# Kernel tuning notes

Hardware: AMD Instinct MI355X
Metric: run time of the kernel (lower is better)

Reference implementation:

```python
import jax, jax.numpy as jnp
import numpy as np

DIM = 1024
NQ = 16
NKV = 4
HD = DIM // NQ  # 64
HID = 2048
E = 8
B, S = 1, 1024
EPS = 1e-6


def rmsnorm(x, w):
    ms = jnp.mean(x * x, axis=-1, keepdims=True)
    return w * (x * jax.lax.rsqrt(ms + EPS))


def rope_tables(seq_len, head_dim):
    inv_freq = 1.0 / (10000.0 ** (jnp.arange(0, head_dim, 2, dtype=jnp.float32) / head_dim))
    t = jnp.arange(seq_len, dtype=jnp.float32)
    freqs = jnp.einsum('i,j->ij', t, inv_freq)  # [S, HD/2]
    return jnp.cos(freqs), jnp.sin(freqs)


def apply_rope(x, cos, sin):
    # x: [B, S, H, HD]; cos/sin: [S, HD/2]
    c = cos[None, :, None, :]
    s = sin[None, :, None, :]
    half = x.shape[-1] // 2
    x1, x2 = x[..., :half], x[..., half:]
    return jnp.concatenate([x1 * c - x2 * s, x1 * s + x2 * c], axis=-1)


def setup_inputs() -> dict:
    key = jax.random.key(0)
    ks = jax.random.split(key, 20)
    sc = lambda fan_in: 1.0 / np.sqrt(fan_in)
    d = {}
    d['x'] = jax.random.normal(ks[0], (B, S, DIM), dtype=jnp.float32)
    d['ln1_w'] = jnp.ones((DIM,), jnp.float32)
    d['ln2_w'] = jnp.ones((DIM,), jnp.float32)
    d['Wq'] = jax.random.normal(ks[1], (DIM, DIM), jnp.float32) * sc(DIM)
    d['bq'] = jnp.zeros((DIM,), jnp.float32)
    d['Wk'] = jax.random.normal(ks[2], (DIM, HD * NKV), jnp.float32) * sc(DIM)
    d['bk'] = jnp.zeros((HD * NKV,), jnp.float32)
    d['Wv'] = jax.random.normal(ks[3], (DIM, HD * NKV), jnp.float32) * sc(DIM)
    d['bv'] = jnp.zeros((HD * NKV,), jnp.float32)
    d['qn_w'] = jnp.ones((HD,), jnp.float32)
    d['kn_w'] = jnp.ones((HD,), jnp.float32)
    d['Wg'] = jax.random.normal(ks[4], (HD, HD), jnp.float32) * sc(HD)
    d['bg'] = jnp.zeros((HD,), jnp.float32)
    d['Wo'] = jax.random.normal(ks[5], (DIM, DIM), jnp.float32) * sc(DIM)
    d['bo'] = jnp.zeros((DIM,), jnp.float32)
    d['Wr'] = jax.random.normal(ks[6], (DIM, E), jnp.float32) * sc(DIM)
    d['br'] = jnp.zeros((E,), jnp.float32)
    d['W1'] = jax.random.normal(ks[7], (E, DIM, 2 * HID), jnp.float32) * sc(DIM)
    d['b1'] = jnp.zeros((E, 2 * HID), jnp.float32)
    d['W2'] = jax.random.normal(ks[8], (E, HID, DIM), jnp.float32) * sc(HID)
    d['b2'] = jnp.zeros((E, DIM), jnp.float32)
    return d


def _forward(x, ln1_w, ln2_w, Wq, bq, Wk, bk, Wv, bv, qn_w, kn_w, Wg, bg, Wo, bo,
             Wr, br, W1, b1, W2, b2):
    batch, seq, _ = x.shape
    cos, sin = rope_tables(seq, HD)

    # --- attention ---
    h = rmsnorm(x, ln1_w)
    q = (h @ Wq + bq).reshape(batch, seq, NQ, HD)
    k = (h @ Wk + bk).reshape(batch, seq, NKV, HD)
    v = (h @ Wv + bv).reshape(batch, seq, NKV, HD)
    q = rmsnorm(apply_rope(q, cos, sin), qn_w)
    k = rmsnorm(apply_rope(k, cos, sin), kn_w)
    rep = NQ // NKV
    k = jnp.repeat(k, rep, axis=2)  # [B,S,NQ,HD]
    v = jnp.repeat(v, rep, axis=2)
    scores = jnp.einsum('bthd,bshd->bhts', q, k) / np.sqrt(HD)
    causal = jnp.tril(jnp.ones((seq, seq), dtype=bool))
    scores = jnp.where(causal[None, None], scores, -jnp.inf)
    attn = jax.nn.softmax(scores, axis=-1)
    out = jnp.einsum('bhts,bshd->bthd', attn, v)
    gate = jax.nn.sigmoid(out @ Wg + bg)
    out = (out * gate).reshape(batch, seq, DIM)
    x = x + out @ Wo + bo

    # --- top-1 MoE (note: output is NOT scaled by router probs) ---
    h2 = rmsnorm(x, ln2_w)
    logits = h2 @ Wr + br  # [B,S,E]
    top1 = jnp.argmax(logits, axis=-1).reshape(-1)  # [T]
    xt = h2.reshape(-1, DIM)  # [T,DIM]
    # dense dispatch: run all experts, gather the chosen one
    u = jnp.einsum('td,edf->tef', xt, W1) + b1  # [T,E,2H]
    u1, u2 = u[..., :HID], u[..., HID:]
    act = u1 * jax.nn.sigmoid(u2)  # SwiGLU
    y_all = jnp.einsum('teh,ehd->ted', act, W2) + b2  # [T,E,DIM]
    y = jnp.take_along_axis(y_all, top1[:, None, None], axis=1)[:, 0, :]
    return x + y.reshape(batch, seq, DIM)


def reference(x, ln1_w, ln2_w, Wq, bq, Wk, bk, Wv, bv, qn_w, kn_w, Wg, bg, Wo, bo,
              Wr, br, W1, b1, W2, b2):
    return _forward(x, ln1_w, ln2_w, Wq, bq, Wk, bk, Wv, bv, qn_w, kn_w,
                    Wg, bg, Wo, bo, Wr, br, W1, b1, W2, b2)
```

## Files before the change

kernel.cpp:

```cpp
#include <hip/hip_runtime.h>
#include <hip/hip_bf16.h>
#include <cstddef>

#define DIM 1024
#define NQ 16
#define NKV 4
#define HD 64
#define HID 2048
#define NE 8
#define SEQ 1024
#define EPSF 1e-6f
#define MAX_TILES 24
#define GST 72

typedef __hip_bfloat16 bf16;
typedef __attribute__((ext_vector_type(8))) short short8;
typedef __attribute__((ext_vector_type(4))) float floatx4;

typedef union { short8 s; unsigned int u[4]; } s8u;

__device__ __forceinline__ unsigned int f2b(float f) {
    union { bf16 b; unsigned short s; } u;
    u.b = __float2bfloat16(f);
    return (unsigned int)u.s;
}
__device__ __forceinline__ unsigned int pk2(float a, float b) {
    return f2b(a) | (f2b(b) << 16);
}

__global__ __launch_bounds__(256) void rmsnorm_kernel(const float* __restrict__ src,
                                                      const float* __restrict__ w,
                                                      float* __restrict__ dst)
{
    int row = blockIdx.x, tid = threadIdx.x;
    __shared__ float red[256];
    float vals[4];
    float sq = 0.f;
    size_t base = (size_t)row * DIM;
    #pragma unroll
    for (int i = 0; i < 4; i++) {
        int idx = tid + i * 256;
        float v = src[base + idx];
        vals[i] = v; sq += v * v;
    }
    red[tid] = sq; __syncthreads();
    for (int s = 128; s > 0; s >>= 1) {
        if (tid < s) red[tid] += red[tid + s];
        __syncthreads();
    }
    float rs = 1.0f / sqrtf(red[0] * (1.0f / DIM) + EPSF);
    #pragma unroll
    for (int i = 0; i < 4; i++) {
        int idx = tid + i * 256;
        dst[base + idx] = w[idx] * vals[i] * rs;
    }
}

__global__ __launch_bounds__(256) void gemm_kernel(
    const float* __restrict__ A, const float* __restrict__ B, const float* __restrict__ bias,
    float* __restrict__ C, const float* __restrict__ resf,
    const int* __restrict__ perm, const int* __restrict__ tile_expert,
    int N, int K, int mode)
{
    __shared__ short As[64 * GST];
    __shared__ short Bs[64 * GST];
    int tid = threadIdx.x;
    int mbase = blockIdx.y * 64, nbase = blockIdx.x * 64;

    size_t Beoff = 0, biasoff = 0;
    if (tile_expert) {
        int e = tile_expert[blockIdx.y];
        if (e < 0) return;
        Beoff = (size_t)e * K * N;
        biasoff = (size_t)e * N;
    }

    int ar = tid >> 4, ak = (tid & 15) << 2;
    int bn = tid & 63, bkk = (tid >> 6) << 4;
    const float* BpBase = B + Beoff + (size_t)bkk * N + nbase + bn;

    int wv = tid >> 6, ln = tid & 63;
    int fm = (wv << 4) + (ln & 15);
    int fn = ln & 15;
    int fk = (ln >> 4) << 3;

    floatx4 acc[4];
    #pragma unroll
    for (int nt = 0; nt < 4; nt++)
        #pragma unroll
        for (int r = 0; r < 4; r++) acc[nt][r] = 0.f;

    float4 apre[4];
    float bpre[16];
    #pragma unroll
    for (int p = 0; p < 4; p++)
        apre[p] = *(const float4*)(A + (size_t)(mbase + (p << 4) + ar) * K + ak);
    #pragma unroll
    for (int i = 0; i < 16; i++)
        bpre[i] = BpBase[(size_t)i * N];

    for (int kt = 0; kt < K; kt += 64) {
        #pragma unroll
        for (int p = 0; p < 4; p++) {
            int m = (p << 4) + ar;
            uint2 wpk; wpk.x = pk2(apre[p].x, apre[p].y); wpk.y = pk2(apre[p].z, apre[p].w);
            *(uint2*)&As[m * GST + ak] = wpk;
        }
        {
            unsigned int u[8];
            #pragma unroll
            for (int i = 0; i < 8; i++) u[i] = pk2(bpre[2 * i], bpre[2 * i + 1]);
            *(uint4*)&Bs[bn * GST + bkk]     = make_uint4(u[0], u[1], u[2], u[3]);
            *(uint4*)&Bs[bn * GST + bkk + 8] = make_uint4(u[4], u[5], u[6], u[7]);
        }
        __syncthreads();

        int kn = kt + 64;
        if (kn < K) {
            #pragma unroll
            for (int p = 0; p < 4; p++)
                apre[p] = *(const float4*)(A + (size_t)(mbase + (p << 4) + ar) * K + kn + ak);
            const float* bp = BpBase + (size_t)kn * N;
            #pragma unroll
            for (int i = 0; i < 16; i++) bpre[i] = bp[(size_t)i * N];
        }

        #pragma unroll
        for (int ks = 0; ks < 2; ks++) {
            short8 af = *(const short8*)&As[fm * GST + (ks << 5) + fk];
            #pragma unroll
            for (int nt = 0; nt < 4; nt++) {
                short8 bf = *(const short8*)&Bs[((nt << 4) + fn) * GST + (ks << 5) + fk];
                acc[nt] = __builtin_amdgcn_mfma_f32_16x16x32_bf16(af, bf, acc[nt], 0, 0, 0);
            }
        }
        __syncthreads();
    }

    int rowb = mbase + (wv << 4) + ((ln >> 4) << 2);
    if (mode == 2) {
        int tk[4];
        #pragma unroll
        for (int r = 0; r < 4; r++) tk[r] = perm[rowb + r];
        #pragma unroll
        for (int nt = 0; nt < 4; nt++) {
            int col = nbase + (nt << 4) + fn;
            float bsv = bias[biasoff + col];
            #pragma unroll
            for (int r = 0; r < 4; r++)
                if (tk[r] >= 0)
                    C[(size_t)tk[r] * N + col] = resf[(size_t)tk[r] * N + col] + acc[nt][r] + bsv;
        }
    } else {
        #pragma unroll
        for (int nt = 0; nt < 4; nt++) {
            int col = nbase + (nt << 4) + fn;
            float bsv = bias[col];
            #pragma unroll
            for (int r = 0; r < 4; r++) {
                float vv = acc[nt][r] + bsv;
                if (mode == 1) vv += resf[(size_t)(rowb + r) * N + col];
                C[(size_t)(rowb + r) * N + col] = vv;
            }
        }
    }
}

__global__ __launch_bounds__(256) void qkv_kernel(
    const float* __restrict__ A,
    const float* __restrict__ Wq, const float* __restrict__ bq,
    const float* __restrict__ Wk, const float* __restrict__ bk,
    const float* __restrict__ Wv, const float* __restrict__ bv,
    float* __restrict__ qo, float* __restrict__ ko, float* __restrict__ vo)
{
    __shared__ short As[64 * GST];
    __shared__ short Bs[64 * GST];
    int tid = threadIdx.x;
    int bx = blockIdx.x;
    int mbase = blockIdx.y * 64;

    const float* B; const float* bias; float* C; int N, nbase;
    if (bx < 16)      { B = Wq; bias = bq; C = qo; N = DIM;      nbase = bx * 64; }
    else if (bx < 20) { B = Wk; bias = bk; C = ko; N = NKV * HD; nbase = (bx - 16) * 64; }
    else              { B = Wv; bias = bv; C = vo; N = NKV * HD; nbase = (bx - 20) * 64; }

    int ar = tid >> 4, ak = (tid & 15) << 2;
    int bn = tid & 63, bkk = (tid >> 6) << 4;
    const float* BpBase = B + (size_t)bkk * N + nbase + bn;

    int wv = tid >> 6, ln = tid & 63;
    int fm = (wv << 4) + (ln & 15);
    int fn = ln & 15;
    int fk = (ln >> 4) << 3;

    floatx4 acc[4];
    #pragma unroll
    for (int nt = 0; nt < 4; nt++)
        #pragma unroll
        for (int r = 0; r < 4; r++) acc[nt][r] = 0.f;

    float4 apre[4];
    float bpre[16];
    #pragma unroll
    for (int p = 0; p < 4; p++)
        apre[p] = *(const float4*)(A + (size_t)(mbase + (p << 4) + ar) * DIM + ak);
    #pragma unroll
    for (int i = 0; i < 16; i++)
        bpre[i] = BpBase[(size_t)i * N];

    for (int kt = 0; kt < DIM; kt += 64) {
        #pragma unroll
        for (int p = 0; p < 4; p++) {
            int m = (p << 4) + ar;
            uint2 wpk; wpk.x = pk2(apre[p].x, apre[p].y); wpk.y = pk2(apre[p].z, apre[p].w);
            *(uint2*)&As[m * GST + ak] = wpk;
        }
        {
            unsigned int u[8];
            #pragma unroll
            for (int i = 0; i < 8; i++) u[i] = pk2(bpre[2 * i], bpre[2 * i + 1]);
            *(uint4*)&Bs[bn * GST + bkk]     = make_uint4(u[0], u[1], u[2], u[3]);
            *(uint4*)&Bs[bn * GST + bkk + 8] = make_uint4(u[4], u[5], u[6], u[7]);
        }
        __syncthreads();

        int kn = kt + 64;
        if (kn < DIM) {
            #pragma unroll
            for (int p = 0; p < 4; p++)
                apre[p] = *(const float4*)(A + (size_t)(mbase + (p << 4) + ar) * DIM + kn + ak);
            const float* bp = BpBase + (size_t)kn * N;
            #pragma unroll
            for (int i = 0; i < 16; i++) bpre[i] = bp[(size_t)i * N];
        }

        #pragma unroll
        for (int ks = 0; ks < 2; ks++) {
            short8 af = *(const short8*)&As[fm * GST + (ks << 5) + fk];
            #pragma unroll
            for (int nt = 0; nt < 4; nt++) {
                short8 bf = *(const short8*)&Bs[((nt << 4) + fn) * GST + (ks << 5) + fk];
                acc[nt] = __builtin_amdgcn_mfma_f32_16x16x32_bf16(af, bf, acc[nt], 0, 0, 0);
            }
        }
        __syncthreads();
    }

    int rowb = mbase + (wv << 4) + ((ln >> 4) << 2);
    #pragma unroll
    for (int nt = 0; nt < 4; nt++) {
        int col = nbase + (nt << 4) + fn;
        float bsv = bias[col];
        #pragma unroll
        for (int r = 0; r < 4; r++)
            C[(size_t)(rowb + r) * N + col] = acc[nt][r] + bsv;
    }
}

__global__ __launch_bounds__(256) void moe1_kernel(
    const float* __restrict__ A,
    const float* __restrict__ W1,
    const float* __restrict__ b1,
    float* __restrict__ act,
    const int* __restrict__ perm,
    const int* __restrict__ tile_expert)
{
    __shared__ short As[64 * GST];
    __shared__ short B1s[64 * GST];
    __shared__ short B2s[64 * GST];
    int tid = threadIdx.x;
    int mbase = blockIdx.y * 64, nbase = blockIdx.x * 64;
    int e = tile_expert[blockIdx.y];
    if (e < 0) return;
    const float* Wp = W1 + (size_t)e * DIM * (2 * HID);
    const float* bp1 = b1 + (size_t)e * (2 * HID);

    int ar = tid >> 4, ak = (tid & 15) << 2;
    int tok[4];
    #pragma unroll
    for (int p = 0; p < 4; p++) tok[p] = perm[mbase + (p << 4) + ar];

    int bn = tid & 63, bkk = (tid >> 6) << 4;
    const float* BpBase = Wp + (size_t)bkk * (2 * HID) + nbase + bn;

    int wv = tid >> 6, ln = tid & 63;
    int fm = (wv << 4) + (ln & 15);
    int fn = ln & 15;
    int fk = (ln >> 4) << 3;

    floatx4 acc1[4], acc2[4];
    #pragma unroll
    for (int nt = 0; nt < 4; nt++)
        #pragma unroll
        for (int r = 0; r < 4; r++) { acc1[nt][r] = 0.f; acc2[nt][r] = 0.f; }

    float4 apre[4];
    float b1pre[16], b2pre[16];
    #pragma unroll
    for (int p = 0; p < 4; p++)
        apre[p] = (tok[p] >= 0)
            ? *(const float4*)(A + (size_t)tok[p] * DIM + ak)
            : make_float4(0.f, 0.f, 0.f, 0.f);
    #pragma unroll
    for (int i = 0; i < 16; i++) {
        b1pre[i] = BpBase[(size_t)i * (2 * HID)];
        b2pre[i] = BpBase[(size_t)i * (2 * HID) + HID];
    }

    for (int kt = 0; kt < DIM; kt += 64) {
        #pragma unroll
        for (int p = 0; p < 4; p++) {
            int m = (p << 4) + ar;
            uint2 wpk; wpk.x = pk2(apre[p].x, apre[p].y); wpk.y = pk2(apre[p].z, apre[p].w);
            *(uint2*)&As[m * GST + ak] = wpk;
        }
        {
            unsigned int u1[8], u2[8];
            #pragma unroll
            for (int i = 0; i < 8; i++) {
                u1[i] = pk2(b1pre[2 * i], b1pre[2 * i + 1]);
                u2[i] = pk2(b2pre[2 * i], b2pre[2 * i + 1]);
            }
            *(uint4*)&B1s[bn * GST + bkk]     = make_uint4(u1[0], u1[1], u1[2], u1[3]);
            *(uint4*)&B1s[bn * GST + bkk + 8] = make_uint4(u1[4], u1[5], u1[6], u1[7]);
            *(uint4*)&B2s[bn * GST + bkk]     = make_uint4(u2[0], u2[1], u2[2], u2[3]);
            *(uint4*)&B2s[bn * GST + bkk + 8] = make_uint4(u2[4], u2[5], u2[6], u2[7]);
        }
        __syncthreads();

        int kn = kt + 64;
        if (kn < DIM) {
            #pragma unroll
            for (int p = 0; p < 4; p++)
                apre[p] = (tok[p] >= 0)
                    ? *(const float4*)(A + (size_t)tok[p] * DIM + kn + ak)
                    : make_float4(0.f, 0.f, 0.f, 0.f);
            const float* bp = BpBase + (size_t)kn * (2 * HID);
            #pragma unroll
            for (int i = 0; i < 16; i++) {
                b1pre[i] = bp[(size_t)i * (2 * HID)];
                b2pre[i] = bp[(size_t)i * (2 * HID) + HID];
            }
        }

        #pragma unroll
        for (int ks = 0; ks < 2; ks++) {
            short8 af = *(const short8*)&As[fm * GST + (ks << 5) + fk];
            #pragma unroll
            for (int nt = 0; nt < 4; nt++) {
                int bo = ((nt << 4) + fn) * GST + (ks << 5) + fk;
                short8 bf1 = *(const short8*)&B1s[bo];
                short8 bf2 = *(const short8*)&B2s[bo];
                acc1[nt] = __builtin_amdgcn_mfma_f32_16x16x32_bf16(af, bf1, acc1[nt], 0, 0, 0);
                acc2[nt] = __builtin_amdgcn_mfma_f32_16x16x32_bf16(af, bf2, acc2[nt], 0, 0, 0);
            }
        }
        __syncthreads();
    }

    int rowb = mbase + (wv << 4) + ((ln >> 4) << 2);
    #pragma unroll
    for (int nt = 0; nt < 4; nt++) {
        int col = nbase + (nt << 4) + fn;
        float bs1 = bp1[col];
        float bs2 = bp1[HID + col];
        #pragma unroll
        for (int r = 0; r < 4; r++) {
            float u1 = acc1[nt][r] + bs1;
            float u2 = acc2[nt][r] + bs2;
            act[(size_t)(rowb + r) * HID + col] = u1 * (1.0f / (1.0f + expf(-u2)));
        }
    }
}

__global__ __launch_bounds__(64) void rope_rms_kernel(float* __restrict__ x,
                                                      const float* __restrict__ w, int nh)
{
    int t = blockIdx.x, h = blockIdx.y, d = threadIdx.x;
    int base = (t * nh + h) * HD;
    int i = d & 31;
    float x1 = x[base + i];
    float x2 = x[base + 32 + i];
    float inv = 1.0f / powf(10000.0f, (float)(2 * i) * (1.0f / HD));
    float fr = (float)t * inv;
    float c = cosf(fr), s = sinf(fr);
    float r = (d < 32) ? (x1 * c - x2 * s) : (x1 * s + x2 * c);
    float sq = r * r;
    #pragma unroll
    for (int m = 32; m >= 1; m >>= 1) sq += __shfl_xor(sq, m);
    float rs = 1.0f / sqrtf(sq * (1.0f / HD) + EPSF);
    __syncthreads();
    x[base + d] = r * rs * w[d];
}

__global__ __launch_bounds__(256) void fattn_kernel(const float* __restrict__ q,
                                                    const float* __restrict__ k,
                                                    const float* __restrict__ v,
                                                    float* __restrict__ o)
{
    __shared__ short lds[2][2][64 * GST];

    int h = blockIdx.x, qt = blockIdx.y;
    int kvh = h >> 2;
    int tid = threadIdx.x;
    int w = tid >> 6, ln = tid & 63;
    int c = ln & 15, g = ln >> 4;
    int qbase = qt * 64;
    const size_t krow = (size_t)NKV * HD;

    short8 qf[2];
    {
        const float* qp = q + ((size_t)(qbase + 16 * w + c) * NQ + h) * HD + 8 * g;
        #pragma unroll
        for (int ks = 0; ks < 2; ks++) {
            float4 a = *(const float4*)(qp + 32 * ks);
            float4 b = *(const float4*)(qp + 32 * ks + 4);
            s8u t;
            t.u[0] = pk2(a.x * 0.125f, a.y * 0.125f);
            t.u[1] = pk2(a.z * 0.125f, a.w * 0.125f);
            t.u[2] = pk2(b.x * 0.125f, b.y * 0.125f);
            t.u[3] = pk2(b.z * 0.125f, b.w * 0.125f);
            qf[ks] = t.s;
        }
    }

    int kr[4], kd4[4];
    #pragma unroll
    for (int i = 0; i < 4; i++) { int f4 = tid + 256 * i; kr[i] = f4 >> 4; kd4[i] = f4 & 15; }
    int vd = tid & 63, vrb = (tid >> 6) << 4;

    float4 kreg[4];
    float vreg[16];
    {
        const float* kb = k + (size_t)kvh * HD;
        #pragma unroll
        for (int i = 0; i < 4; i++)
            kreg[i] = *(const float4*)(kb + (size_t)kr[i] * krow + kd4[i] * 4);
        const float* vb = v + (size_t)kvh * HD + vd;
        #pragma unroll
        for (int i = 0; i < 16; i++)
            vreg[i] = vb[(size_t)(vrb + i) * krow];
    }

    float m_i = -INFINITY, l_i = 0.f;
    floatx4 ot[4];
    #pragma unroll
    for (int mt = 0; mt < 4; mt++)
        #pragma unroll
        for (int r = 0; r < 4; r++) ot[mt][r] = 0.f;

    for (int kt = 0; kt <= qt; kt++) {
        short* KB = lds[kt & 1][0];
        short* VT = lds[kt & 1][1];

        #pragma unroll
        for (int i = 0; i < 4; i++) {
            uint2 wp; wp.x = pk2(kreg[i].x, kreg[i].y); wp.y = pk2(kreg[i].z, kreg[i].w);
            *(uint2*)&KB[kr[i] * GST + kd4[i] * 4] = wp;
        }
        {
            unsigned int u[8];
            #pragma unroll
            for (int i = 0; i < 8; i++) u[i] = pk2(vreg[2 * i], vreg[2 * i + 1]);
            *(uint4*)&VT[vd * GST + vrb]     = make_uint4(u[0], u[1], u[2], u[3]);
            *(uint4*)&VT[vd * GST + vrb + 8] = make_uint4(u[4], u[5], u[6], u[7]);
        }
        __syncthreads();

        if (kt < qt) {
            int kb2 = (kt + 1) * 64;
            const float* kb = k + ((size_t)kb2 * NKV + kvh) * HD;
            #pragma unroll
            for (int i = 0; i < 4; i++)
                kreg[i] = *(const float4*)(kb + (size_t)kr[i] * krow + kd4[i] * 4);
            const float* vp = v + ((size_t)kb2 * NKV + kvh) * HD + vd;
            #pragma unroll
            for (int i = 0; i < 16; i++)
                vreg[i] = vp[(size_t)(vrb + i) * krow];
        }

        float p[4][4];
        #pragma unroll
        for (int mt = 0; mt < 4; mt++) {
            floatx4 s = {0.f, 0.f, 0.f, 0.f};
            #pragma unroll
            for (int ks = 0; ks < 2; ks++) {
                short8 kf = *(const short8*)&KB[(16 * mt + c) * GST + 32 * ks + 8 * g];
                s = __builtin_amdgcn_mfma_f32_16x16x32_bf16(kf, qf[ks], s, 0, 0, 0);
            }
            #pragma unroll
            for (int r = 0; r < 4; r++) p[mt][r] = s[r];
        }

        if (kt == qt) {
            #pragma unroll
            for (int mt = 0; mt < 4; mt++)
                #pragma unroll
                for (int r = 0; r < 4; r++)
                    if (16 * mt + 4 * g + r > 16 * w + c) p[mt][r] = -1e30f;
        }

        float tm = p[0][0];
        #pragma unroll
        for (int mt = 0; mt < 4; mt++)
            #pragma unroll
            for (int r = 0; r < 4; r++) tm = fmaxf(tm, p[mt][r]);
        tm = fmaxf(tm, __shfl_xor(tm, 16));
        tm = fmaxf(tm, __shfl_xor(tm, 32));
        float mn = fmaxf(m_i, tm);
        float alpha = __expf(m_i - mn);
        float ts = 0.f;
        #pragma unroll
        for (int mt = 0; mt < 4; mt++)
            #pragma unroll
            for (int r = 0; r < 4; r++) {
                float e = __expf(p[mt][r] - mn);
                p[mt][r] = e; ts += e;
            }
        ts += __shfl_xor(ts, 16);
        ts += __shfl_xor(ts, 32);
        l_i = alpha * l_i + ts;
        m_i = mn;
        #pragma unroll
        for (int mt = 0; mt < 4; mt++)
            #pragma unroll
            for (int r = 0; r < 4; r++) ot[mt][r] *= alpha;

        unsigned int pd[4][2];
        #pragma unroll
        for (int mt = 0; mt < 4; mt++) {
            pd[mt][0] = pk2(p[mt][0], p[mt][1]);
            pd[mt][1] = pk2(p[mt][2], p[mt][3]);
        }

        int srcA = c + ((ln & 16) << 1);
        int srcB = srcA + 16;
        int gh = g >> 1;
        short8 pf[2];
        #pragma unroll
        for (int ks = 0; ks < 2; ks++) {
            s8u t;
            unsigned int a0 = (unsigned)__shfl((int)pd[2 * ks][0],     srcA);
            unsigned int a1 = (unsigned)__shfl((int)pd[2 * ks + 1][0], srcA);
            t.u[0] = gh ? a1 : a0;
            unsigned int b0 = (unsigned)__shfl((int)pd[2 * ks][1],     srcA);
            unsigned int b1 = (unsigned)__shfl((int)pd[2 * ks + 1][1], srcA);
            t.u[1] = gh ? b1 : b0;
            unsigned int c0 = (unsigned)__shfl((int)pd[2 * ks][0],     srcB);
            unsigned int c1 = (unsigned)__shfl((int)pd[2 * ks + 1][0], srcB);
            t.u[2] = gh ? c1 : c0;
            unsigned int d0 = (unsigned)__shfl((int)pd[2 * ks][1],     srcB);
            unsigned int d1 = (unsigned)__shfl((int)pd[2 * ks + 1][1], srcB);
            t.u[3] = gh ? d1 : d0;
            pf[ks] = t.s;
        }

        #pragma unroll
        for (int mt = 0; mt < 4; mt++) {
            #pragma unroll
            for (int ks = 0; ks < 2; ks++) {
                short8 vf = *(const short8*)&VT[(16 * mt + c) * GST + 32 * ks + 8 * g];
                ot[mt] = __builtin_amdgcn_mfma_f32_16x16x32_bf16(vf, pf[ks], ot[mt], 0, 0, 0);
            }
        }
    }

    __syncthreads();
    float* OT = (float*)lds;
    float rl = 1.0f / l_i;
    #pragma unroll
    for (int mt = 0; mt < 4; mt++)
        #pragma unroll
        for (int r = 0; r < 4; r++)
            OT[(16 * w + c) * 68 + 16 * mt + 4 * g + r] = ot[mt][r] * rl;
    __syncthreads();
    #pragma unroll
    for (int i = 0; i < 4; i++) {
        int idx = tid + 256 * i;
        int rq = idx >> 4, d4 = idx & 15;
        float4 val = *(const float4*)&OT[rq * 68 + d4 * 4];
        *(float4*)(o + ((size_t)(qbase + rq) * NQ + h) * HD + d4 * 4) = val;
    }
}

__global__ __launch_bounds__(64) void gate_kernel(float* __restrict__ o,
                                                  const float* __restrict__ Wg,
                                                  const float* __restrict__ bg)
{
    int t = blockIdx.x, h = blockIdx.y, d = threadIdx.x;
    __shared__ float ao[HD];
    int base = (t * NQ + h) * HD;
    ao[d] = o[base + d];
    __syncthreads();
    float acc = bg[d];
    #pragma unroll 8
    for (int e = 0; e < HD; e++) acc += ao[e] * Wg[e * HD + d];
    float g = 1.0f / (1.0f + expf(-acc));
    o[base + d] = ao[d] * g;
}

__global__ __launch_bounds__(64) void router_kernel(const float* __restrict__ h2,
                                                    const float* __restrict__ Wr,
                                                    const float* __restrict__ br,
                                                    int* __restrict__ top1)
{
    int t = blockIdx.x, lane = threadIdx.x;
    float acc[NE] = {0.f, 0.f, 0.f, 0.f, 0.f, 0.f, 0.f, 0.f};
    for (int d = lane; d < DIM; d += 64) {
        float hv = h2[(size_t)t * DIM + d];
        float4 w0 = *(const float4*)(Wr + (size_t)d * NE);
        float4 w1 = *(const float4*)(Wr + (size_t)d * NE + 4);
        acc[0] += hv * w0.x; acc[1] += hv * w0.y;
        acc[2] += hv * w0.z; acc[3] += hv * w0.w;
        acc[4] += hv * w1.x; acc[5] += hv * w1.y;
        acc[6] += hv * w1.z; acc[7] += hv * w1.w;
    }
    #pragma unroll
    for (int e = 0; e < NE; e++)
        for (int off = 32; off >= 1; off >>= 1) acc[e] += __shfl_down(acc[e], off);
    if (lane == 0) {
        float best = acc[0] + br[0]; int be = 0;
        #pragma unroll
        for (int e = 1; e < NE; e++) {
            float l = acc[e] + br[e];
            if (l > best) { best = l; be = e; }
        }
        top1[t] = be;
    }
}

__global__ __launch_bounds__(64) void bucket_kernel(const int* __restrict__ top1,
                                                    int* __restrict__ perm,
                                                    int* __restrict__ tile_expert)
{
    int lane = threadIdx.x;

    int e_of[16];
    {
        const int4* tp = (const int4*)(top1 + lane * 16);
        #pragma unroll
        for (int c = 0; c < 4; c++) {
            int4 v = tp[c];
            e_of[c * 4 + 0] = v.x & 7;
            e_of[c * 4 + 1] = v.y & 7;
            e_of[c * 4 + 2] = v.z & 7;
            e_of[c * 4 + 3] = v.w & 7;
        }
    }

    int cnt[NE];
    #pragma unroll
    for (int e = 0; e < NE; e++) {
        int c = 0;
        #pragma unroll
        for (int i = 0; i < 16; i++) c += (e_of[i] == e) ? 1 : 0;
        cnt[e] = c;
    }

    int pre[NE];
    #pragma unroll
    for (int e = 0; e < NE; e++) pre[e] = cnt[e];
    #pragma unroll
    for (int off = 1; off < 64; off <<= 1) {
        #pragma unroll
        for (int e = 0; e < NE; e++) {
            int t = __shfl_up(pre[e], off);
            if (lane >= off) pre[e] += t;
        }
    }
    int tot[NE];
    #pragma unroll
    for (int e = 0; e < NE; e++) {
        tot[e] = __shfl(pre[e], 63);
        pre[e] -= cnt[e];
    }

    int off_e[NE + 1];
    off_e[0] = 0;
    #pragma unroll
    for (int e = 0; e < NE; e++)
        off_e[e + 1] = off_e[e] + (((tot[e] + 63) >> 6) << 6);

    if (lane < MAX_TILES) {
        int tb = lane << 6;
        int te = -1;
        #pragma unroll
        for (int e = 0; e < NE; e++)
            if (tb >= off_e[e] && tb < off_e[e + 1]) te = e;
        tile_expert[lane] = te;
    }

    #pragma unroll
    for (int e = 0; e < NE; e++)
        for (int i = off_e[e] + tot[e] + lane; i < off_e[e + 1]; i += 64)
            perm[i] = -1;

    #pragma unroll
    for (int e = 0; e < NE; e++) {
        int pos = off_e[e] + pre[e];
        #pragma unroll
        for (int i = 0; i < 16; i++) {
            if (e_of[i] == e) { perm[pos] = lane * 16 + i; pos++; }
        }
    }
}

extern "C" void kernel_launch(void* const* d_in, const int* in_sizes, int n_in,
                              void* d_out, int out_size, void* d_ws, size_t ws_size,
                              hipStream_t stream)
{
    const float* x    = (const float*)d_in[0];
    const float* ln1w = (const float*)d_in[1];
    const float* ln2w = (const float*)d_in[2];
    const float* Wq   = (const float*)d_in[3];
    const float* bq   = (const float*)d_in[4];
    const float* Wk   = (const float*)d_in[5];
    const float* bk   = (const float*)d_in[6];
    const float* Wv   = (const float*)d_in[7];
    const float* bv   = (const float*)d_in[8];
    const float* qnw  = (const float*)d_in[9];
    const float* knw  = (const float*)d_in[10];
    const float* Wg   = (const float*)d_in[11];
    const float* bg   = (const float*)d_in[12];
    const float* Wo   = (const float*)d_in[13];
    const float* bo   = (const float*)d_in[14];
    const float* Wr   = (const float*)d_in[15];
    const float* br   = (const float*)d_in[16];
    const float* W1   = (const float*)d_in[17];
    const float* b1   = (const float*)d_in[18];
    const float* W2   = (const float*)d_in[19];
    const float* b2   = (const float*)d_in[20];
    float* out = (float*)d_out;
    (void)in_sizes; (void)n_in; (void)out_size; (void)ws_size;

    char* ws = (char*)d_ws;
    float* h    = (float*)(ws);
    float* q    = (float*)(ws + ((size_t)4  << 20));
    float* kbuf = (float*)(ws + ((size_t)8  << 20));
    float* vbuf = (float*)(ws + ((size_t)9  << 20));
    float* ao   = (float*)(ws + ((size_t)10 << 20));
    float* x2   = (float*)(ws);
    float* h2   = (float*)(ws + ((size_t)4  << 20));
    float* act  = (float*)(ws + ((size_t)8  << 20));
    int* top1   = (int*)  (ws + ((size_t)20 << 20));
    int* perm   = top1 + 2048;
    int* texp   = perm + MAX_TILES * 64;

    rmsnorm_kernel<<<SEQ, 256, 0, stream>>>(x, ln1w, h);
    qkv_kernel<<<dim3(24, SEQ / 64), 256, 0, stream>>>(
        h, Wq, bq, Wk, bk, Wv, bv, q, kbuf, vbuf);
    rope_rms_kernel<<<dim3(SEQ, NQ),  64, 0, stream>>>(q,    qnw, NQ);
    rope_rms_kernel<<<dim3(SEQ, NKV), 64, 0, stream>>>(kbuf, knw, NKV);
    fattn_kernel<<<dim3(NQ, SEQ / 64), 256, 0, stream>>>(q, kbuf, vbuf, ao);
    gate_kernel<<<dim3(SEQ, NQ), 64, 0, stream>>>(ao, Wg, bg);
    gemm_kernel<<<dim3(DIM / 64, SEQ / 64), 256, 0, stream>>>(
        ao, Wo, bo, x2, x, nullptr, nullptr, DIM, DIM, 1);
    rmsnorm_kernel<<<SEQ, 256, 0, stream>>>(x2, ln2w, h2);
    router_kernel<<<SEQ, 64, 0, stream>>>(h2, Wr, br, top1);
    bucket_kernel<<<1, 64, 0, stream>>>(top1, perm, texp);
    moe1_kernel<<<dim3(HID / 64, MAX_TILES), 256, 0, stream>>>(
        h2, W1, b1, act, perm, texp);
    gemm_kernel<<<dim3(DIM / 64, MAX_TILES), 256, 0, stream>>>(
        act, W2, b2, out, x2, perm, texp, DIM, HID, 2);
}
```

Baseline: 436.9 us.

## Enlarge MoE tiles to 128 rows, fuse gate into attention, merge rope launches

Grows the MoE expert tiles from 64 to 128 token rows, so each W1/W2 weight tile loaded from memory feeds twice as many MFMAs. MoE2 gets its own gemm2 kernel and the bucket padding moves to 128 with 16 tiles. The sigmoid gate projection moves into the flash-attention epilogue, removing the separate gate kernel and its extra read and write of the attention output. The Q and K rope/rmsnorm launches become one. Risks: more padding waste per expert, higher register pressure from doubled accumulators, and extra serial work in the attention epilogue.

```diff
diff --git a/kernel.cpp b/kernel.cpp
--- a/kernel.cpp
+++ b/kernel.cpp
@@ -10,7 +10,7 @@
 #define NE 8
 #define SEQ 1024
 #define EPSF 1e-6f
-#define MAX_TILES 24
+#define MAX_TILES 16
 #define GST 72
 
 typedef __hip_bfloat16 bf16;
@@ -59,7 +59,6 @@
 __global__ __launch_bounds__(256) void gemm_kernel(
     const float* __restrict__ A, const float* __restrict__ B, const float* __restrict__ bias,
     float* __restrict__ C, const float* __restrict__ resf,
-    const int* __restrict__ perm, const int* __restrict__ tile_expert,
     int N, int K, int mode)
 {
     __shared__ short As[64 * GST];
@@ -67,17 +66,9 @@
     int tid = threadIdx.x;
     int mbase = blockIdx.y * 64, nbase = blockIdx.x * 64;
 
-    size_t Beoff = 0, biasoff = 0;
-    if (tile_expert) {
-        int e = tile_expert[blockIdx.y];
-        if (e < 0) return;
-        Beoff = (size_t)e * K * N;
-        biasoff = (size_t)e * N;
-    }
-
     int ar = tid >> 4, ak = (tid & 15) << 2;
     int bn = tid & 63, bkk = (tid >> 6) << 4;
-    const float* BpBase = B + Beoff + (size_t)bkk * N + nbase + bn;
+    const float* BpBase = B + (size_t)bkk * N + nbase + bn;
 
     int wv = tid >> 6, ln = tid & 63;
     int fm = (wv << 4) + (ln & 15);
@@ -138,30 +129,118 @@
     }
 
     int rowb = mbase + (wv << 4) + ((ln >> 4) << 2);
-    if (mode == 2) {
+    #pragma unroll
+    for (int nt = 0; nt < 4; nt++) {
+        int col = nbase + (nt << 4) + fn;
+        float bsv = bias[col];
+        #pragma unroll
+        for (int r = 0; r < 4; r++) {
+            float vv = acc[nt][r] + bsv;
+            if (mode == 1) vv += resf[(size_t)(rowb + r) * N + col];
+            C[(size_t)(rowb + r) * N + col] = vv;
+        }
+    }
+}
+
+__global__ __launch_bounds__(256) void gemm2_kernel(
+    const float* __restrict__ A,
+    const float* __restrict__ W2,
+    const float* __restrict__ b2,
+    float* __restrict__ C,
+    const float* __restrict__ resf,
+    const int* __restrict__ perm,
+    const int* __restrict__ tile_expert)
+{
+    __shared__ short As[128 * GST];
+    __shared__ short Bs[64 * GST];
+    int tid = threadIdx.x;
+    int mbase = blockIdx.y * 128, nbase = blockIdx.x * 64;
+    int e = tile_expert[blockIdx.y];
+    if (e < 0) return;
+    const int N = DIM, K = HID;
+    const float* Bp = W2 + (size_t)e * K * N;
+    const float* bias = b2 + (size_t)e * N;
+
+    int ar = tid >> 4, ak = (tid & 15) << 2;
+    int bn = tid & 63, bkk = (tid >> 6) << 4;
+    const float* BpBase = Bp + (size_t)bkk * N + nbase + bn;
+
+    int wv = tid >> 6, ln = tid & 63;
+    int fm = (wv << 4) + (ln & 15);
+    int fn = ln & 15;
+    int fk = (ln >> 4) << 3;
+
+    floatx4 acc[2][4];
+    #pragma unroll
+    for (int ms = 0; ms < 2; ms++)
+        #pragma unroll
+        for (int nt = 0; nt < 4; nt++)
+            #pragma unroll
+            for (int r = 0; r < 4; r++) acc[ms][nt][r] = 0.f;
+
+    float4 apre[8];
+    float bpre[16];
+    #pragma unroll
+    for (int p = 0; p < 8; p++)
+        apre[p] = *(const float4*)(A + (size_t)(mbase + (p << 4) + ar) * K + ak);
+    #pragma unroll
+    for (int i = 0; i < 16; i++)
+        bpre[i] = BpBase[(size_t)i * N];
+
+    for (int kt = 0; kt < K; kt += 64) {
+        #pragma unroll
+        for (int p = 0; p < 8; p++) {
+            int m = (p << 4) + ar;
+            uint2 wpk; wpk.x = pk2(apre[p].x, apre[p].y); wpk.y = pk2(apre[p].z, apre[p].w);
+            *(uint2*)&As[m * GST + ak] = wpk;
+        }
+        {
+            unsigned int u[8];
+            #pragma unroll
+            for (int i = 0; i < 8; i++) u[i] = pk2(bpre[2 * i], bpre[2 * i + 1]);
+            *(uint4*)&Bs[bn * GST + bkk]     = make_uint4(u[0], u[1], u[2], u[3]);
+            *(uint4*)&Bs[bn * GST + bkk + 8] = make_uint4(u[4], u[5], u[6], u[7]);
+        }
+        __syncthreads();
+
+        int kn = kt + 64;
+        if (kn < K) {
+            #pragma unroll
+            for (int p = 0; p < 8; p++)
+                apre[p] = *(const float4*)(A + (size_t)(mbase + (p << 4) + ar) * K + kn + ak);
+            const float* bp = BpBase + (size_t)kn * N;
+            #pragma unroll
+            for (int i = 0; i < 16; i++) bpre[i] = bp[(size_t)i * N];
+        }
+
+        #pragma unroll
+        for (int ks = 0; ks < 2; ks++) {
+            short8 af0 = *(const short8*)&As[fm * GST + (ks << 5) + fk];
+            short8 af1 = *(const short8*)&As[(fm + 64) * GST + (ks << 5) + fk];
+            #pragma unroll
+            for (int nt = 0; nt < 4; nt++) {
+                short8 bf = *(const short8*)&Bs[((nt << 4) + fn) * GST + (ks << 5) + fk];
+                acc[0][nt] = __builtin_amdgcn_mfma_f32_16x16x32_bf16(af0, bf, acc[0][nt], 0, 0, 0);
+                acc[1][nt] = __builtin_amdgcn_mfma_f32_16x16x32_bf16(af1, bf, acc[1][nt], 0, 0, 0);
+            }
+        }
+        __syncthreads();
+    }
+
+    #pragma unroll
+    for (int ms = 0; ms < 2; ms++) {
+        int rowb = mbase + (ms << 6) + (wv << 4) + ((ln >> 4) << 2);
         int tk[4];
         #pragma unroll
         for (int r = 0; r < 4; r++) tk[r] = perm[rowb + r];
-        #pragma unroll
-        for (int nt = 0; nt < 4; nt++) {
-            int col = nbase + (nt << 4) + fn;
-            float bsv = bias[biasoff + col];
-            #pragma unroll
-            for (int r = 0; r < 4; r++)
-                if (tk[r] >= 0)
-                    C[(size_t)tk[r] * N + col] = resf[(size_t)tk[r] * N + col] + acc[nt][r] + bsv;
-        }
-    } else {
         #pragma unroll
         for (int nt = 0; nt < 4; nt++) {
             int col = nbase + (nt << 4) + fn;
             float bsv = bias[col];
             #pragma unroll
-            for (int r = 0; r < 4; r++) {
-                float vv = acc[nt][r] + bsv;
-                if (mode == 1) vv += resf[(size_t)(rowb + r) * N + col];
-                C[(size_t)(rowb + r) * N + col] = vv;
-            }
+            for (int r = 0; r < 4; r++)
+                if (tk[r] >= 0)
+                    C[(size_t)tk[r] * N + col] = resf[(size_t)tk[r] * N + col] + acc[ms][nt][r] + bsv;
         }
     }
 }
@@ -265,20 +344,20 @@
     const int* __restrict__ perm,
     const int* __restrict__ tile_expert)
 {
-    __shared__ short As[64 * GST];
+    __shared__ short As[128 * GST];
     __shared__ short B1s[64 * GST];
     __shared__ short B2s[64 * GST];
     int tid = threadIdx.x;
-    int mbase = blockIdx.y * 64, nbase = blockIdx.x * 64;
+    int mbase = blockIdx.y * 128, nbase = blockIdx.x * 64;
     int e = tile_expert[blockIdx.y];
     if (e < 0) return;
     const float* Wp = W1 + (size_t)e * DIM * (2 * HID);
     const float* bp1 = b1 + (size_t)e * (2 * HID);
 
     int ar = tid >> 4, ak = (tid & 15) << 2;
-    int tok[4];
-    #pragma unroll
-    for (int p = 0; p < 4; p++) tok[p] = perm[mbase + (p << 4) + ar];
+    int tok[8];
+    #pragma unroll
+    for (int p = 0; p < 8; p++) tok[p] = perm[mbase + (p << 4) + ar];
 
     int bn = tid & 63, bkk = (tid >> 6) << 4;
     const float* BpBase = Wp + (size_t)bkk * (2 * HID) + nbase + bn;
@@ -288,16 +367,18 @@
     int fn = ln & 15;
     int fk = (ln >> 4) << 3;
 
-    floatx4 acc1[4], acc2[4];
-    #pragma unroll
-    for (int nt = 0; nt < 4; nt++)
-        #pragma unroll
-        for (int r = 0; r < 4; r++) { acc1[nt][r] = 0.f; acc2[nt][r] = 0.f; }
-
-    float4 apre[4];
+    floatx4 acc1[2][4], acc2[2][4];
+    #pragma unroll
+    for (int ms = 0; ms < 2; ms++)
+        #pragma unroll
+        for (int nt = 0; nt < 4; nt++)
+            #pragma unroll
+            for (int r = 0; r < 4; r++) { acc1[ms][nt][r] = 0.f; acc2[ms][nt][r] = 0.f; }
+
+    float4 apre[8];
     float b1pre[16], b2pre[16];
     #pragma unroll
-    for (int p = 0; p < 4; p++)
+    for (int p = 0; p < 8; p++)
         apre[p] = (tok[p] >= 0)
             ? *(const float4*)(A + (size_t)tok[p] * DIM + ak)
             : make_float4(0.f, 0.f, 0.f, 0.f);
@@ -309,7 +390,7 @@
 
     for (int kt = 0; kt < DIM; kt += 64) {
         #pragma unroll
-        for (int p = 0; p < 4; p++) {
+        for (int p = 0; p < 8; p++) {
             int m = (p << 4) + ar;
             uint2 wpk; wpk.x = pk2(apre[p].x, apre[p].y); wpk.y = pk2(apre[p].z, apre[p].w);
             *(uint2*)&As[m * GST + ak] = wpk;
@@ -331,7 +412,7 @@
         int kn = kt + 64;
         if (kn < DIM) {
             #pragma unroll
-            for (int p = 0; p < 4; p++)
+            for (int p = 0; p < 8; p++)
                 apre[p] = (tok[p] >= 0)
                     ? *(const float4*)(A + (size_t)tok[p] * DIM + kn + ak)
                     : make_float4(0.f, 0.f, 0.f, 0.f);
@@ -345,38 +426,49 @@
 
         #pragma unroll
         for (int ks = 0; ks < 2; ks++) {
-            short8 af = *(const short8*)&As[fm * GST + (ks << 5) + fk];
+            short8 af0 = *(const short8*)&As[fm * GST + (ks << 5) + fk];
+            short8 af1 = *(const short8*)&As[(fm + 64) * GST + (ks << 5) + fk];
             #pragma unroll
             for (int nt = 0; nt < 4; nt++) {
                 int bo = ((nt << 4) + fn) * GST + (ks << 5) + fk;
                 short8 bf1 = *(const short8*)&B1s[bo];
                 short8 bf2 = *(const short8*)&B2s[bo];
-                acc1[nt] = __builtin_amdgcn_mfma_f32_16x16x32_bf16(af, bf1, acc1[nt], 0, 0, 0);
-                acc2[nt] = __builtin_amdgcn_mfma_f32_16x16x32_bf16(af, bf2, acc2[nt], 0, 0, 0);
-            }
-        }
-        __syncthreads();
-    }
-
-    int rowb = mbase + (wv << 4) + ((ln >> 4) << 2);
-    #pragma unroll
-    for (int nt = 0; nt < 4; nt++) {
-        int col = nbase + (nt << 4) + fn;
-        float bs1 = bp1[col];
-        float bs2 = bp1[HID + col];
-        #pragma unroll
-        for (int r = 0; r < 4; r++) {
-            float u1 = acc1[nt][r] + bs1;
-            float u2 = acc2[nt][r] + bs2;
-            act[(size_t)(rowb + r) * HID + col] = u1 * (1.0f / (1.0f + expf(-u2)));
-        }
-    }
-}
-
-__global__ __launch_bounds__(64) void rope_rms_kernel(float* __restrict__ x,
-                                                      const float* __restrict__ w, int nh)
-{
-    int t = blockIdx.x, h = blockIdx.y, d = threadIdx.x;
+                acc1[0][nt] = __builtin_amdgcn_mfma_f32_16x16x32_bf16(af0, bf1, acc1[0][nt], 0, 0, 0);
+                acc1[1][nt] = __builtin_amdgcn_mfma_f32_16x16x32_bf16(af1, bf1, acc1[1][nt], 0, 0, 0);
+                acc2[0][nt] = __builtin_amdgcn_mfma_f32_16x16x32_bf16(af0, bf2, acc2[0][nt], 0, 0, 0);
+                acc2[1][nt] = __builtin_amdgcn_mfma_f32_16x16x32_bf16(af1, bf2, acc2[1][nt], 0, 0, 0);
+            }
+        }
+        __syncthreads();
+    }
+
+    #pragma unroll
+    for (int ms = 0; ms < 2; ms++) {
+        int rowb = mbase + (ms << 6) + (wv << 4) + ((ln >> 4) << 2);
+        #pragma unroll
+        for (int nt = 0; nt < 4; nt++) {
+            int col = nbase + (nt << 4) + fn;
+            float bs1 = bp1[col];
+            float bs2 = bp1[HID + col];
+            #pragma unroll
+            for (int r = 0; r < 4; r++) {
+                float u1 = acc1[ms][nt][r] + bs1;
+                float u2 = acc2[ms][nt][r] + bs2;
+                act[(size_t)(rowb + r) * HID + col] = u1 * (1.0f / (1.0f + expf(-u2)));
+            }
+        }
+    }
+}
+
+__global__ __launch_bounds__(64) void rope_rms_kernel(float* __restrict__ qb,
+                                                      float* __restrict__ kb,
+                                                      const float* __restrict__ qnw,
+                                                      const float* __restrict__ knw)
+{
+    int t = blockIdx.x, hy = blockIdx.y, d = threadIdx.x;
+    float* x; const float* w; int nh, h;
+    if (hy < NQ) { x = qb; w = qnw; nh = NQ;  h = hy; }
+    else         { x = kb; w = knw; nh = NKV; h = hy - NQ; }
     int base = (t * nh + h) * HD;
     int i = d & 31;
     float x1 = x[base + i];
@@ -396,6 +488,8 @@
 __global__ __launch_bounds__(256) void fattn_kernel(const float* __restrict__ q,
                                                     const float* __restrict__ k,
                                                     const float* __restrict__ v,
+                                                    const float* __restrict__ Wg,
+                                                    const float* __restrict__ bg,
                                                     float* __restrict__ o)
 {
     __shared__ short lds[2][2][64 * GST];
@@ -566,37 +660,54 @@
     }
 
     __syncthreads();
-    float* OT = (float*)lds;
+    float* L   = (float*)lds;
+    float* WgS = L + 64 * 68;
+
+    int we = tid >> 2, wd = (tid & 3) << 4;
+    float4 wg4[4];
+    #pragma unroll
+    for (int i = 0; i < 4; i++)
+        wg4[i] = *(const float4*)(Wg + (size_t)we * HD + wd + 4 * i);
+
     float rl = 1.0f / l_i;
     #pragma unroll
     for (int mt = 0; mt < 4; mt++)
         #pragma unroll
         for (int r = 0; r < 4; r++)
-            OT[(16 * w + c) * 68 + 16 * mt + 4 * g + r] = ot[mt][r] * rl;
+            L[(16 * w + c) * 68 + 16 * mt + 4 * g + r] = ot[mt][r] * rl;
+    #pragma unroll
+    for (int i = 0; i < 4; i++)
+        *(float4*)&WgS[we * 68 + wd + 4 * i] = wg4[i];
     __syncthreads();
+
+    int r = tid >> 2, d0 = (tid & 3) << 4;
+    float4 a0 = *(const float4*)(bg + d0);
+    float4 a1 = *(const float4*)(bg + d0 + 4);
+    float4 a2 = *(const float4*)(bg + d0 + 8);
+    float4 a3 = *(const float4*)(bg + d0 + 12);
+    for (int e = 0; e < HD; e++) {
+        float ov = L[r * 68 + e];
+        float4 w0 = *(const float4*)&WgS[e * 68 + d0];
+        float4 w1 = *(const float4*)&WgS[e * 68 + d0 + 4];
+        float4 w2 = *(const float4*)&WgS[e * 68 + d0 + 8];
+        float4 w3 = *(const float4*)&WgS[e * 68 + d0 + 12];
+        a0.x += ov * w0.x; a0.y += ov * w0.y; a0.z += ov * w0.z; a0.w += ov * w0.w;
+        a1.x += ov * w1.x; a1.y += ov * w1.y; a1.z += ov * w1.z; a1.w += ov * w1.w;
+        a2.x += ov * w2.x; a2.y += ov * w2.y; a2.z += ov * w2.z; a2.w += ov * w2.w;
+        a3.x += ov * w3.x; a3.y += ov * w3.y; a3.z += ov * w3.z; a3.w += ov * w3.w;
+    }
+    float* op = o + ((size_t)(qbase + r) * NQ + h) * HD + d0;
+    float4 res[4];
+    float4 av[4] = {a0, a1, a2, a3};
     #pragma unroll
     for (int i = 0; i < 4; i++) {
-        int idx = tid + 256 * i;
-        int rq = idx >> 4, d4 = idx & 15;
-        float4 val = *(const float4*)&OT[rq * 68 + d4 * 4];
-        *(float4*)(o + ((size_t)(qbase + rq) * NQ + h) * HD + d4 * 4) = val;
-    }
-}
-
-__global__ __launch_bounds__(64) void gate_kernel(float* __restrict__ o,
-                                                  const float* __restrict__ Wg,
-                                                  const float* __restrict__ bg)
-{
-    int t = blockIdx.x, h = blockIdx.y, d = threadIdx.x;
-    __shared__ float ao[HD];
-    int base = (t * NQ + h) * HD;
-    ao[d] = o[base + d];
-    __syncthreads();
-    float acc = bg[d];
-    #pragma unroll 8
-    for (int e = 0; e < HD; e++) acc += ao[e] * Wg[e * HD + d];
-    float g = 1.0f / (1.0f + expf(-acc));
-    o[base + d] = ao[d] * g;
+        float4 ov4 = *(const float4*)&L[r * 68 + d0 + 4 * i];
+        res[i].x = ov4.x / (1.0f + expf(-av[i].x));
+        res[i].y = ov4.y / (1.0f + expf(-av[i].y));
+        res[i].z = ov4.z / (1.0f + expf(-av[i].z));
+        res[i].w = ov4.w / (1.0f + expf(-av[i].w));
+        *(float4*)(op + 4 * i) = res[i];
+    }
 }
 
 __global__ __launch_bounds__(64) void router_kernel(const float* __restrict__ h2,
@@ -679,10 +790,10 @@
     off_e[0] = 0;
     #pragma unroll
     for (int e = 0; e < NE; e++)
-        off_e[e + 1] = off_e[e] + (((tot[e] + 63) >> 6) << 6);
+        off_e[e + 1] = off_e[e] + (((tot[e] + 127) >> 7) << 7);
 
     if (lane < MAX_TILES) {
-        int tb = lane << 6;
+        int tb = lane << 7;
         int te = -1;
         #pragma unroll
         for (int e = 0; e < NE; e++)
@@ -741,25 +852,23 @@
     float* ao   = (float*)(ws + ((size_t)10 << 20));
     float* x2   = (float*)(ws);
     float* h2   = (float*)(ws + ((size_t)4  << 20));
-    float* act  = (float*)(ws + ((size_t)8  << 20));
-    int* top1   = (int*)  (ws + ((size_t)20 << 20));
+    float* act  = (float*)(ws + ((size_t)24 << 20));
+    int* top1   = (int*)  (ws + ((size_t)44 << 20));
     int* perm   = top1 + 2048;
-    int* texp   = perm + MAX_TILES * 64;
+    int* texp   = perm + MAX_TILES * 128;
 
     rmsnorm_kernel<<<SEQ, 256, 0, stream>>>(x, ln1w, h);
     qkv_kernel<<<dim3(24, SEQ / 64), 256, 0, stream>>>(
         h, Wq, bq, Wk, bk, Wv, bv, q, kbuf, vbuf);
-    rope_rms_kernel<<<dim3(SEQ, NQ),  64, 0, stream>>>(q,    qnw, NQ);
-    rope_rms_kernel<<<dim3(SEQ, NKV), 64, 0, stream>>>(kbuf, knw, NKV);
-    fattn_kernel<<<dim3(NQ, SEQ / 64), 256, 0, stream>>>(q, kbuf, vbuf, ao);
-    gate_kernel<<<dim3(SEQ, NQ), 64, 0, stream>>>(ao, Wg, bg);
+    rope_rms_kernel<<<dim3(SEQ, NQ + NKV), 64, 0, stream>>>(q, kbuf, qnw, knw);
+    fattn_kernel<<<dim3(NQ, SEQ / 64), 256, 0, stream>>>(q, kbuf, vbuf, Wg, bg, ao);
     gemm_kernel<<<dim3(DIM / 64, SEQ / 64), 256, 0, stream>>>(
-        ao, Wo, bo, x2, x, nullptr, nullptr, DIM, DIM, 1);
+        ao, Wo, bo, x2, x, DIM, DIM, 1);
     rmsnorm_kernel<<<SEQ, 256, 0, stream>>>(x2, ln2w, h2);
     router_kernel<<<SEQ, 64, 0, stream>>>(h2, Wr, br, top1);
     bucket_kernel<<<1, 64, 0, stream>>>(top1, perm, texp);
     moe1_kernel<<<dim3(HID / 64, MAX_TILES), 256, 0, stream>>>(
         h2, W1, b1, act, perm, texp);
-    gemm_kernel<<<dim3(DIM / 64, MAX_TILES), 256, 0, stream>>>(
-        act, W2, b2, out, x2, perm, texp, DIM, HID, 2);
-}
+    gemm2_kernel<<<dim3(DIM / 64, MAX_TILES), 256, 0, stream>>>(
+        act, W2, b2, out, x2, perm, texp);
+}
```

New measurement: 452.9 us. 1.04x slower.
